# Kernel tuning notes

Hardware: AMD Instinct MI355X
Metric: run time of the kernel (lower is better)

Reference implementation:

```python
import jax, jax.numpy as jnp
import numpy as np

NUM_HEADS = 8
GROUPS = 32
EPS = 1e-5


def group_norm(x, gamma, beta):
    # x: (b, c, L)
    b, c, L = x.shape
    xg = x.reshape(b, GROUPS, c // GROUPS, L)
    mean = xg.mean(axis=(2, 3), keepdims=True)
    var = xg.var(axis=(2, 3), keepdims=True)
    xn = ((xg - mean) / jnp.sqrt(var + EPS)).reshape(b, c, L)
    return xn * gamma[None, :, None] + beta[None, :, None]


def setup_inputs() -> dict:
    key = jax.random.key(0)
    ks = jax.random.split(key, 8)
    b, c, h, w = 8, 512, 32, 32
    inner = c  # inner_channels == -1 -> channels
    x = jax.random.normal(ks[0], (b, c, h, w), dtype=jnp.float32)
    gamma = jnp.ones((c,), dtype=jnp.float32)
    beta = jnp.zeros((c,), dtype=jnp.float32)
    Wq = jax.random.normal(ks[1], (inner, c), dtype=jnp.float32) * 0.02
    bq = jnp.zeros((inner,), dtype=jnp.float32)
    Wkv = jax.random.normal(ks[2], (2 * inner, c), dtype=jnp.float32) * 0.02
    bkv = jnp.zeros((2 * inner,), dtype=jnp.float32)
    Wo = jax.random.normal(ks[3], (c, inner), dtype=jnp.float32) * 0.02
    bo = jnp.zeros((c,), dtype=jnp.float32)
    return {"x": x, "gamma": gamma, "beta": beta, "Wq": Wq, "bq": bq,
            "Wkv": Wkv, "bkv": bkv, "Wo": Wo, "bo": bo}


def reference(x, gamma, beta, Wq, bq, Wkv, bkv, Wo, bo):
    b, c = x.shape[:2]
    spatial = x.shape[2:]
    L = int(np.prod(spatial))
    inner = Wq.shape[0]
    dh = inner // NUM_HEADS
    scale = dh ** -0.5  # NOTE: applied to BOTH q and k, as in the source

    xr = x.reshape(b, c, L)
    hn = group_norm(xr, gamma, beta)          # norm(x); also serves as context

    # 1x1 Conv1d == channel matmul
    q = jnp.einsum('oc,bcl->bol', Wq, hn) + bq[None, :, None]
    kv = jnp.einsum('oc,bcl->bol', Wkv, hn) + bkv[None, :, None]
    k, v = jnp.split(kv, 2, axis=1)

    # (b, heads, dh, L)
    qh = (q * scale).reshape(b, NUM_HEADS, dh, L)
    kh = (k * scale).reshape(b, NUM_HEADS, dh, L)
    vh = v.reshape(b, NUM_HEADS, dh, L)

    dots = jnp.einsum('bhdt,bhds->bhts', qh, kh)
    attn = jax.nn.softmax(dots.astype(jnp.float32), axis=-1).astype(dots.dtype)
    out = jnp.einsum('bhts,bhds->bhdt', attn, vh)  # (b, heads, dh, L)

    out = out.reshape(b, inner, L)
    # output Linear over the channel dim
    out = jnp.einsum('oc,bcl->bol', Wo, out) + bo[None, :, None]
    return (xr + out).reshape(b, c, *spatial)
```

## Files before the change

### kernel.cpp

```cpp
#include <hip/hip_runtime.h>
#include <math.h>

#define B_ 8
#define C_ 512
#define L_ 1024
#define NH_ 8
#define DH_ 64
#define EPS 1e-5f
#define SCALE 0.125f
#define QSCALE (0.125f * 1.44269504088896f)

typedef __bf16 bf16x8 __attribute__((ext_vector_type(8)));
typedef __bf16 bf16x4 __attribute__((ext_vector_type(4)));
typedef float  f32x4  __attribute__((ext_vector_type(4)));

#define MFMA16(a, b, c) __builtin_amdgcn_mfma_f32_16x16x32_bf16((a), (b), (c), 0, 0, 0)

__device__ __forceinline__ void glds16(const __bf16* g, __bf16* l) {
    __builtin_amdgcn_global_load_lds((const __attribute__((address_space(1))) void*)(g),
                                     (__attribute__((address_space(3))) void*)(l),
                                     16, 0, 0);
}

__global__ __launch_bounds__(256)
void prep_kernel(const float* __restrict__ Wq, const float* __restrict__ Wkv,
                 const float* __restrict__ Wo, __bf16* __restrict__ dst,
                 const float* __restrict__ x, float* __restrict__ stats) {
    __shared__ float rs[256], rss[256];
    int bid = blockIdx.x, tid = threadIdx.x;
    if (bid < 1024) {
        int idx = bid * 256 + tid;
        float4 v;
        if (idx < 65536)        v = ((const float4*)Wq)[idx];
        else if (idx < 196608)  v = ((const float4*)Wkv)[idx - 65536];
        else                    v = ((const float4*)Wo)[idx - 196608];
        bf16x4 o;
        o[0] = (__bf16)v.x; o[1] = (__bf16)v.y; o[2] = (__bf16)v.z; o[3] = (__bf16)v.w;
        ((bf16x4*)dst)[idx] = o;
        return;
    }
    int bg = bid - 1024;
    size_t goff = (size_t)bg * 16 * L_;
    const float4* x4 = (const float4*)(x + goff);
    float s = 0.f, ss = 0.f;
    for (int i = tid; i < 4096; i += 256) {
        float4 v = x4[i];
        s  += v.x + v.y + v.z + v.w;
        ss += v.x * v.x + v.y * v.y + v.z * v.z + v.w * v.w;
    }
    rs[tid] = s; rss[tid] = ss;
    __syncthreads();
    for (int off = 128; off > 0; off >>= 1) {
        if (tid < off) { rs[tid] += rs[tid + off]; rss[tid] += rss[tid + off]; }
        __syncthreads();
    }
    if (tid == 0) {
        const float inv_n = 1.f / 16384.f;
        float mean = rs[0] * inv_n;
        float var  = rss[0] * inv_n - mean * mean;
        stats[bg * 2]     = mean;
        stats[bg * 2 + 1] = rsqrtf(var + EPS);
    }
}

__global__ __launch_bounds__(256)
void gn_apply_kernel(const float* __restrict__ x, const float* __restrict__ gamma,
                     const float* __restrict__ beta, const float* __restrict__ stats,
                     __bf16* __restrict__ hnT) {
    __shared__ __bf16 T[32 * 520];
    const int lt = blockIdx.x, b = blockIdx.y;
    const int tid = threadIdx.x;
    const int l0 = lt * 32;
    const int cbase = tid >> 3, fl = tid & 7;
#pragma unroll
    for (int p = 0; p < 16; ++p) {
        int cc = cbase + p * 32;
        float4 v = *(const float4*)&x[((size_t)b * C_ + cc) * L_ + l0 + fl * 4];
        int bg = b * 32 + (cc >> 4);
        float m = stats[bg * 2], rstd = stats[bg * 2 + 1];
        float ga = gamma[cc] * rstd, be = beta[cc];
        T[(fl * 4 + 0) * 520 + cc] = (__bf16)((v.x - m) * ga + be);
        T[(fl * 4 + 1) * 520 + cc] = (__bf16)((v.y - m) * ga + be);
        T[(fl * 4 + 2) * 520 + cc] = (__bf16)((v.z - m) * ga + be);
        T[(fl * 4 + 3) * 520 + cc] = (__bf16)((v.w - m) * ga + be);
    }
    __syncthreads();
    const int lrow = tid >> 6, cu = tid & 63;
#pragma unroll
    for (int pp = 0; pp < 8; ++pp) {
        int l = pp * 4 + lrow;
        bf16x8 r = *(const bf16x8*)&T[l * 520 + cu * 8];
        *(bf16x8*)&hnT[((size_t)b * L_ + l0 + l) * C_ + cu * 8] = r;
    }
}

__device__ __forceinline__
void gemm_mainloop(const __bf16* __restrict__ A, const __bf16* __restrict__ Bp,
                   __bf16* As, __bf16* Bs, f32x4 acc[4][4]) {
    const int tid = threadIdx.x;
    const int lane = tid & 63, w = tid >> 6;
    const int c = lane & 15, q = lane >> 4;
    const int wm = (w >> 1) * 64, wn = (w & 1) * 64;
    const int l8 = lane >> 3, kgsw = (lane & 7) ^ l8;

    for (int k0 = 0; k0 < 512; k0 += 64) {
#pragma unroll
        for (int i = 0; i < 4; ++i) {
            int chunk = w * 4 + i;
            int row = chunk * 8 + l8;
            glds16(A  + (size_t)row * 512 + k0 + kgsw * 8, &As[chunk * 512]);
            glds16(Bp + (size_t)row * 512 + k0 + kgsw * 8, &Bs[chunk * 512]);
        }
        __syncthreads();
#pragma unroll
        for (int ks = 0; ks < 2; ++ks) {
            const int koff = ((ks * 4 + q) ^ (c & 7)) * 8;
            bf16x8 af[4], bfr[4];
#pragma unroll
            for (int m = 0; m < 4; ++m)
                af[m] = *(const bf16x8*)&As[(wm + m * 16 + c) * 64 + koff];
#pragma unroll
            for (int n = 0; n < 4; ++n)
                bfr[n] = *(const bf16x8*)&Bs[(wn + n * 16 + c) * 64 + koff];
#pragma unroll
            for (int m = 0; m < 4; ++m)
#pragma unroll
                for (int n = 0; n < 4; ++n)
                    acc[m][n] = MFMA16(af[m], bfr[n], acc[m][n]);
        }
        __syncthreads();
    }
}

__global__ __launch_bounds__(256)
void qkv_kernel(const __bf16* __restrict__ Wq_bf, const __bf16* __restrict__ Wkv_bf,
                const __bf16* __restrict__ hnT,
                const float* __restrict__ bq, const float* __restrict__ bkv,
                __bf16* __restrict__ qT, __bf16* __restrict__ kT,
                __bf16* __restrict__ vv) {
    __shared__ __bf16 SMEM[128 * 64 * 2];
    __bf16* As = SMEM;
    __bf16* Bs = SMEM + 128 * 64;
    const int b = blockIdx.y;
    const int xx = blockIdx.x;
    const int sec = xx >> 5, t = xx & 31;
    const __bf16* hb = hnT + (size_t)b * L_ * C_;

    const __bf16 *A, *Bp;
    int m0, n0;
    if (sec < 2) {
        m0 = (t & 3) * 128; n0 = (t >> 2) * 128;
        A  = (sec == 0 ? Wq_bf : Wkv_bf) + (size_t)m0 * 512;
        Bp = hb + (size_t)n0 * 512;
    } else {
        m0 = (t >> 2) * 128; n0 = (t & 3) * 128;
        A  = hb + (size_t)m0 * 512;
        Bp = Wkv_bf + (size_t)(512 + n0) * 512;
    }

    f32x4 acc[4][4];
#pragma unroll
    for (int m = 0; m < 4; ++m)
#pragma unroll
        for (int n = 0; n < 4; ++n)
#pragma unroll
            for (int r = 0; r < 4; ++r) acc[m][n][r] = 0.f;

    gemm_mainloop(A, Bp, As, Bs, acc);

    const int tid = threadIdx.x, lane = tid & 63, w = tid >> 6;
    const int c = lane & 15, q = lane >> 4;
    const int wm = (w >> 1) * 64, wn = (w & 1) * 64;

    __bf16* T2 = SMEM;
    const float* bias = (sec == 0) ? bq : bkv;
    const float scl = (sec == 0) ? QSCALE : SCALE;
#pragma unroll
    for (int mt = 0; mt < 4; ++mt)
#pragma unroll
        for (int nt = 0; nt < 4; ++nt) {
            int n_loc = wn + nt * 16 + c;
            int u4 = (wm >> 2) + mt * 4 + q;
            int u4sw = u4 ^ ((n_loc & 7) << 1);
            bf16x4 ov;
            if (sec < 2) {
                int ob = m0 + wm + mt * 16 + q * 4;
#pragma unroll
                for (int r = 0; r < 4; ++r)
                    ov[r] = (__bf16)((acc[mt][nt][r] + bias[ob + r]) * scl);
            } else {
                float bi = bkv[512 + n0 + n_loc];
#pragma unroll
                for (int r = 0; r < 4; ++r)
                    ov[r] = (__bf16)(acc[mt][nt][r] + bi);
            }
            *(bf16x4*)&T2[n_loc * 128 + u4sw * 4] = ov;
        }
    __syncthreads();
#pragma unroll
    for (int p = 0; p < 8; ++p) {
        int rrow = p * 16 + (tid >> 4);
        int u16 = tid & 15;
        int u4p = (u16 * 2) ^ ((rrow & 7) << 1);
        bf16x8 val = *(const bf16x8*)&T2[rrow * 128 + u4p * 4];
        if (sec < 2) {
            int l = n0 + rrow;
            int og = m0 + u16 * 8;
            int hh = og >> 6, d0 = og & 63;
            __bf16* dstp = (sec == 0) ? qT : kT;
            *(bf16x8*)&dstp[((size_t)(b * NH_ + hh) * L_ + l) * DH_ + d0] = val;
        } else {
            int o = n0 + rrow;
            int lg = m0 + u16 * 8;
            *(bf16x8*)&vv[((size_t)b * C_ + o) * L_ + lg] = val;
        }
    }
}

__global__ __launch_bounds__(256)
void attn_kernel(const __bf16* __restrict__ qT, const __bf16* __restrict__ kT,
                 const __bf16* __restrict__ vv, __bf16* __restrict__ aoT) {
    const int tt = blockIdx.x, h = blockIdx.y, b = blockIdx.z;
    const int t0 = tt * 128;
    __shared__ __bf16 Qs[128 * 64];
    __shared__ __bf16 Ks[64 * 64];
    __shared__ __bf16 Vs[64 * 64];
    __shared__ __bf16 Ones[16 * 64];
    __shared__ __bf16 Ps[128 * 72];

    const int tid = threadIdx.x, lane = tid & 63, w = tid >> 6;
    const int c = lane & 15, q = lane >> 4;
    const int l8 = lane >> 3, kg = (lane & 7) ^ l8;

    const __bf16* qbase = qT + ((size_t)(b * NH_ + h) * L_ + t0) * DH_;
    const __bf16* kbase = kT + (size_t)(b * NH_ + h) * L_ * DH_;
    const __bf16* vbase = vv + (size_t)(b * C_ + h * DH_) * L_;

    {
        int row = tid >> 4, u8 = tid & 15;
        int u8sw = (((u8 >> 1) ^ (row & 7)) << 1) | (u8 & 1);
        float fv = (row == 0) ? 1.f : 0.f;
        bf16x4 val;
        val[0] = (__bf16)fv; val[1] = (__bf16)fv; val[2] = (__bf16)fv; val[3] = (__bf16)fv;
        *(bf16x4*)&Ones[row * 64 + u8sw * 4] = val;
    }
#pragma unroll
    for (int i = 0; i < 4; ++i) {
        int chunk = w * 4 + i;
        int row = chunk * 8 + l8;
        glds16(qbase + (size_t)row * DH_ + kg * 8, &Qs[chunk * 512]);
    }

    f32x4 o_acc[2][4], o_l[2];
#pragma unroll
    for (int n2 = 0; n2 < 2; ++n2) {
#pragma unroll
        for (int dt = 0; dt < 4; ++dt)
#pragma unroll
            for (int r = 0; r < 4; ++r) o_acc[n2][dt][r] = 0.f;
#pragma unroll
        for (int r = 0; r < 4; ++r) o_l[n2][r] = 0.f;
    }

    for (int s0 = 0; s0 < L_; s0 += 64) {
#pragma unroll
        for (int i = 0; i < 2; ++i) {
            int chunk = w * 2 + i;
            int row = chunk * 8 + l8;
            glds16(kbase + (size_t)(s0 + row) * DH_ + kg * 8, &Ks[chunk * 512]);
            glds16(vbase + (size_t)row * L_ + s0 + kg * 8, &Vs[chunk * 512]);
        }
        __syncthreads();

        f32x4 sres[4][2];
#pragma unroll
        for (int mt = 0; mt < 4; ++mt)
#pragma unroll
            for (int r = 0; r < 4; ++r) { sres[mt][0][r] = 0.f; sres[mt][1][r] = 0.f; }
#pragma unroll
        for (int ks = 0; ks < 2; ++ks) {
            const int koff = ((ks * 4 + q) ^ (c & 7)) * 8;
            bf16x8 bQ0 = *(const bf16x8*)&Qs[(w * 32 + c) * 64 + koff];
            bf16x8 bQ1 = *(const bf16x8*)&Qs[(w * 32 + 16 + c) * 64 + koff];
#pragma unroll
            for (int mt = 0; mt < 4; ++mt) {
                bf16x8 aK = *(const bf16x8*)&Ks[(mt * 16 + c) * 64 + koff];
                sres[mt][0] = MFMA16(aK, bQ0, sres[mt][0]);
                sres[mt][1] = MFMA16(aK, bQ1, sres[mt][1]);
            }
        }

#pragma unroll
        for (int n2 = 0; n2 < 2; ++n2) {
            int trow = w * 32 + n2 * 16 + c;
#pragma unroll
            for (int mt = 0; mt < 4; ++mt) {
                bf16x4 pv;
#pragma unroll
                for (int r = 0; r < 4; ++r) pv[r] = (__bf16)exp2f(sres[mt][n2][r]);
                *(bf16x4*)&Ps[trow * 72 + (mt * 4 + q) * 4] = pv;
            }
        }

#pragma unroll
        for (int ks = 0; ks < 2; ++ks) {
            const int koff = ((ks * 4 + q) ^ (c & 7)) * 8;
            bf16x8 aV[4];
#pragma unroll
            for (int dt = 0; dt < 4; ++dt)
                aV[dt] = *(const bf16x8*)&Vs[(dt * 16 + c) * 64 + koff];
            bf16x8 aO = *(const bf16x8*)&Ones[c * 64 + koff];
#pragma unroll
            for (int n2 = 0; n2 < 2; ++n2) {
                bf16x8 bp = *(const bf16x8*)&Ps[(w * 32 + n2 * 16 + c) * 72 + ks * 32 + q * 8];
#pragma unroll
                for (int dt = 0; dt < 4; ++dt)
                    o_acc[n2][dt] = MFMA16(aV[dt], bp, o_acc[n2][dt]);
                o_l[n2] = MFMA16(aO, bp, o_l[n2]);
            }
        }
        __syncthreads();
    }

#pragma unroll
    for (int n2 = 0; n2 < 2; ++n2) {
        float lsum = __shfl(o_l[n2][0], c);
        float linv = 1.f / lsum;
        int tg = t0 + w * 32 + n2 * 16 + c;
        __bf16* aobase = aoT + ((size_t)b * L_ + tg) * C_ + h * DH_;
#pragma unroll
        for (int dt = 0; dt < 4; ++dt) {
            bf16x4 ov;
#pragma unroll
            for (int r = 0; r < 4; ++r) ov[r] = (__bf16)(o_acc[n2][dt][r] * linv);
            *(bf16x4*)&aobase[dt * 16 + q * 4] = ov;
        }
    }
}

__global__ __launch_bounds__(256)
void proj_kernel(const __bf16* __restrict__ aoT, const __bf16* __restrict__ Wo_bf,
                 const float* __restrict__ bo, const float* __restrict__ x,
                 float* __restrict__ out) {
    __shared__ __bf16 As[128 * 64], Bs[128 * 64];
    const int b = blockIdx.y, t = blockIdx.x;
    const int m0 = (t >> 2) * 128;
    const int n0 = (t & 3) * 128;
    const __bf16* A  = aoT + (size_t)b * L_ * C_ + (size_t)m0 * 512;
    const __bf16* Bp = Wo_bf + (size_t)n0 * 512;

    f32x4 acc[4][4];
#pragma unroll
    for (int m = 0; m < 4; ++m)
#pragma unroll
        for (int n = 0; n < 4; ++n)
#pragma unroll
            for (int r = 0; r < 4; ++r) acc[m][n][r] = 0.f;

    gemm_mainloop(A, Bp, As, Bs, acc);

    const int tid = threadIdx.x, lane = tid & 63, w = tid >> 6;
    const int c = lane & 15, q = lane >> 4;
    const int wm = (w >> 1) * 64, wn = (w & 1) * 64;

#pragma unroll
    for (int mt = 0; mt < 4; ++mt)
#pragma unroll
        for (int nt = 0; nt < 4; ++nt) {
            int lb = m0 + wm + mt * 16 + q * 4;
            int o  = n0 + wn + nt * 16 + c;
            float bi = bo[o];
            size_t off = ((size_t)b * C_ + o) * L_ + lb;
            float4 xv = *(const float4*)&x[off];
            float4 rv;
            rv.x = acc[mt][nt][0] + bi + xv.x;
            rv.y = acc[mt][nt][1] + bi + xv.y;
            rv.z = acc[mt][nt][2] + bi + xv.z;
            rv.w = acc[mt][nt][3] + bi + xv.w;
            *(float4*)&out[off] = rv;
        }
}

extern "C" void kernel_launch(void* const* d_in, const int* in_sizes, int n_in,
                              void* d_out, int out_size, void* d_ws, size_t ws_size,
                              hipStream_t stream) {
    const float* x     = (const float*)d_in[0];
    const float* gamma = (const float*)d_in[1];
    const float* beta  = (const float*)d_in[2];
    const float* Wq    = (const float*)d_in[3];
    const float* bq    = (const float*)d_in[4];
    const float* Wkv   = (const float*)d_in[5];
    const float* bkv   = (const float*)d_in[6];
    const float* Wo    = (const float*)d_in[7];
    const float* bo    = (const float*)d_in[8];
    float* out = (float*)d_out;

    __bf16* wsb = (__bf16*)d_ws;
    __bf16* Wq_bf  = wsb;
    __bf16* Wkv_bf = wsb + 262144;
    __bf16* Wo_bf  = wsb + 786432;
    __bf16* hnT    = wsb + 1048576;
    __bf16* qT     = wsb + 5242880;
    __bf16* kT     = wsb + 9437184;
    __bf16* vv     = wsb + 13631488;
    __bf16* aoT    = wsb + 17825792;
    float*  stats  = (float*)(wsb + 22020096);

    prep_kernel<<<dim3(1280), 256, 0, stream>>>(Wq, Wkv, Wo, wsb, x, stats);
    gn_apply_kernel<<<dim3(32, B_), 256, 0, stream>>>(x, gamma, beta, stats, hnT);
    qkv_kernel<<<dim3(96, B_), 256, 0, stream>>>(Wq_bf, Wkv_bf, hnT, bq, bkv, qT, kT, vv);
    attn_kernel<<<dim3(8, NH_, B_), 256, 0, stream>>>(qT, kT, vv, aoT);
    proj_kernel<<<dim3(32, B_), 256, 0, stream>>>(aoT, Wo_bf, bo, x, out);
}
```

Baseline: 174.3 us.

## Double-buffer K/V tiles in attention and use 512 threads with 16 query rows per wave

The attention kernel now runs 8 waves per block, each handling 16 query rows instead of 32, and double-buffers the K and V LDS tiles so the load of tile it+2 is issued while tile it is being computed. Raw s_waitcnt/s_barrier asm replaces __syncthreads to keep one tile's loads in flight. The aim is to hide global-load latency and raise wave-level parallelism, at the cost of more LDS, more barrier traffic and K/V fragments that are no longer reused across two query subtiles per wave.

```diff
diff --git a/kernel.cpp b/kernel.cpp
--- a/kernel.cpp
+++ b/kernel.cpp
@@ -217,14 +217,14 @@
     }
 }
 
-__global__ __launch_bounds__(256)
+__global__ __launch_bounds__(512)
 void attn_kernel(const __bf16* __restrict__ qT, const __bf16* __restrict__ kT,
                  const __bf16* __restrict__ vv, __bf16* __restrict__ aoT) {
     const int tt = blockIdx.x, h = blockIdx.y, b = blockIdx.z;
     const int t0 = tt * 128;
     __shared__ __bf16 Qs[128 * 64];
-    __shared__ __bf16 Ks[64 * 64];
-    __shared__ __bf16 Vs[64 * 64];
+    __shared__ __bf16 Ks[2][64 * 64];
+    __shared__ __bf16 Vs[2][64 * 64];
     __shared__ __bf16 Ones[16 * 64];
     __shared__ __bf16 Ps[128 * 72];
 
@@ -236,7 +236,7 @@
     const __bf16* kbase = kT + (size_t)(b * NH_ + h) * L_ * DH_;
     const __bf16* vbase = vv + (size_t)(b * C_ + h * DH_) * L_;
 
-    {
+    if (tid < 256) {
         int row = tid >> 4, u8 = tid & 15;
         int u8sw = (((u8 >> 1) ^ (row & 7)) << 1) | (u8 & 1);
         float fv = (row == 0) ? 1.f : 0.f;
@@ -245,59 +245,56 @@
         *(bf16x4*)&Ones[row * 64 + u8sw * 4] = val;
     }
 #pragma unroll
-    for (int i = 0; i < 4; ++i) {
-        int chunk = w * 4 + i;
+    for (int i = 0; i < 2; ++i) {
+        int chunk = w * 2 + i;
         int row = chunk * 8 + l8;
         glds16(qbase + (size_t)row * DH_ + kg * 8, &Qs[chunk * 512]);
     }
-
-    f32x4 o_acc[2][4], o_l[2];
-#pragma unroll
-    for (int n2 = 0; n2 < 2; ++n2) {
-#pragma unroll
-        for (int dt = 0; dt < 4; ++dt)
-#pragma unroll
-            for (int r = 0; r < 4; ++r) o_acc[n2][dt][r] = 0.f;
-#pragma unroll
-        for (int r = 0; r < 4; ++r) o_l[n2][r] = 0.f;
-    }
-
-    for (int s0 = 0; s0 < L_; s0 += 64) {
-#pragma unroll
-        for (int i = 0; i < 2; ++i) {
-            int chunk = w * 2 + i;
-            int row = chunk * 8 + l8;
-            glds16(kbase + (size_t)(s0 + row) * DH_ + kg * 8, &Ks[chunk * 512]);
-            glds16(vbase + (size_t)row * L_ + s0 + kg * 8, &Vs[chunk * 512]);
-        }
-        __syncthreads();
-
-        f32x4 sres[4][2];
+    {
+        int row = w * 8 + l8;
+        glds16(kbase + (size_t)row * DH_ + kg * 8, &Ks[0][w * 512]);
+        glds16(vbase + (size_t)row * L_ + kg * 8, &Vs[0][w * 512]);
+        glds16(kbase + (size_t)(64 + row) * DH_ + kg * 8, &Ks[1][w * 512]);
+        glds16(vbase + (size_t)row * L_ + 64 + kg * 8, &Vs[1][w * 512]);
+    }
+    asm volatile("s_waitcnt vmcnt(2) lgkmcnt(0)" ::: "memory");
+    asm volatile("s_barrier" ::: "memory");
+
+    f32x4 o_acc[4], o_l;
+#pragma unroll
+    for (int dt = 0; dt < 4; ++dt)
+#pragma unroll
+        for (int r = 0; r < 4; ++r) o_acc[dt][r] = 0.f;
+#pragma unroll
+    for (int r = 0; r < 4; ++r) o_l[r] = 0.f;
+
+    for (int it = 0; it < 16; ++it) {
+        const __bf16* Kc = Ks[it & 1];
+        const __bf16* Vc = Vs[it & 1];
+
+        f32x4 sres[4];
 #pragma unroll
         for (int mt = 0; mt < 4; ++mt)
 #pragma unroll
-            for (int r = 0; r < 4; ++r) { sres[mt][0][r] = 0.f; sres[mt][1][r] = 0.f; }
+            for (int r = 0; r < 4; ++r) sres[mt][r] = 0.f;
 #pragma unroll
         for (int ks = 0; ks < 2; ++ks) {
             const int koff = ((ks * 4 + q) ^ (c & 7)) * 8;
-            bf16x8 bQ0 = *(const bf16x8*)&Qs[(w * 32 + c) * 64 + koff];
-            bf16x8 bQ1 = *(const bf16x8*)&Qs[(w * 32 + 16 + c) * 64 + koff];
+            bf16x8 bQ = *(const bf16x8*)&Qs[(w * 16 + c) * 64 + koff];
 #pragma unroll
             for (int mt = 0; mt < 4; ++mt) {
-                bf16x8 aK = *(const bf16x8*)&Ks[(mt * 16 + c) * 64 + koff];
-                sres[mt][0] = MFMA16(aK, bQ0, sres[mt][0]);
-                sres[mt][1] = MFMA16(aK, bQ1, sres[mt][1]);
+                bf16x8 aK = *(const bf16x8*)&Kc[(mt * 16 + c) * 64 + koff];
+                sres[mt] = MFMA16(aK, bQ, sres[mt]);
             }
         }
 
-#pragma unroll
-        for (int n2 = 0; n2 < 2; ++n2) {
-            int trow = w * 32 + n2 * 16 + c;
+        {
+            int trow = w * 16 + c;
 #pragma unroll
             for (int mt = 0; mt < 4; ++mt) {
                 bf16x4 pv;
 #pragma unroll
-                for (int r = 0; r < 4; ++r) pv[r] = (__bf16)exp2f(sres[mt][n2][r]);
+                for (int r = 0; r < 4; ++r) pv[r] = (__bf16)exp2f(sres[mt][r]);
                 *(bf16x4*)&Ps[trow * 72 + (mt * 4 + q) * 4] = pv;
             }
         }
@@ -305,34 +302,39 @@
 #pragma unroll
         for (int ks = 0; ks < 2; ++ks) {
             const int koff = ((ks * 4 + q) ^ (c & 7)) * 8;
-            bf16x8 aV[4];
-#pragma unroll
-            for (int dt = 0; dt < 4; ++dt)
-                aV[dt] = *(const bf16x8*)&Vs[(dt * 16 + c) * 64 + koff];
+            bf16x8 bp = *(const bf16x8*)&Ps[(w * 16 + c) * 72 + ks * 32 + q * 8];
             bf16x8 aO = *(const bf16x8*)&Ones[c * 64 + koff];
 #pragma unroll
-            for (int n2 = 0; n2 < 2; ++n2) {
-                bf16x8 bp = *(const bf16x8*)&Ps[(w * 32 + n2 * 16 + c) * 72 + ks * 32 + q * 8];
-#pragma unroll
-                for (int dt = 0; dt < 4; ++dt)
-                    o_acc[n2][dt] = MFMA16(aV[dt], bp, o_acc[n2][dt]);
-                o_l[n2] = MFMA16(aO, bp, o_l[n2]);
+            for (int dt = 0; dt < 4; ++dt) {
+                bf16x8 aV = *(const bf16x8*)&Vc[(dt * 16 + c) * 64 + koff];
+                o_acc[dt] = MFMA16(aV, bp, o_acc[dt]);
             }
-        }
-        __syncthreads();
-    }
-
-#pragma unroll
-    for (int n2 = 0; n2 < 2; ++n2) {
-        float lsum = __shfl(o_l[n2][0], c);
+            o_l = MFMA16(aO, bp, o_l);
+        }
+
+        asm volatile("s_barrier" ::: "memory");
+        if (it < 14) {
+            int s0n = (it + 2) * 64;
+            int row = w * 8 + l8;
+            glds16(kbase + (size_t)(s0n + row) * DH_ + kg * 8, &Ks[it & 1][w * 512]);
+            glds16(vbase + (size_t)row * L_ + s0n + kg * 8, &Vs[it & 1][w * 512]);
+            asm volatile("s_waitcnt vmcnt(2)" ::: "memory");
+        } else {
+            asm volatile("s_waitcnt vmcnt(0)" ::: "memory");
+        }
+        asm volatile("s_barrier" ::: "memory");
+    }
+
+    {
+        float lsum = __shfl(o_l[0], c);
         float linv = 1.f / lsum;
-        int tg = t0 + w * 32 + n2 * 16 + c;
+        int tg = t0 + w * 16 + c;
         __bf16* aobase = aoT + ((size_t)b * L_ + tg) * C_ + h * DH_;
 #pragma unroll
         for (int dt = 0; dt < 4; ++dt) {
             bf16x4 ov;
 #pragma unroll
-            for (int r = 0; r < 4; ++r) ov[r] = (__bf16)(o_acc[n2][dt][r] * linv);
+            for (int r = 0; r < 4; ++r) ov[r] = (__bf16)(o_acc[dt][r] * linv);
             *(bf16x4*)&aobase[dt * 16 + q * 4] = ov;
         }
     }
@@ -409,6 +411,6 @@
     prep_kernel<<<dim3(1280), 256, 0, stream>>>(Wq, Wkv, Wo, wsb, x, stats);
     gn_apply_kernel<<<dim3(32, B_), 256, 0, stream>>>(x, gamma, beta, stats, hnT);
     qkv_kernel<<<dim3(96, B_), 256, 0, stream>>>(Wq_bf, Wkv_bf, hnT, bq, bkv, qT, kT, vv);
-    attn_kernel<<<dim3(8, NH_, B_), 256, 0, stream>>>(qT, kT, vv, aoT);
+    attn_kernel<<<dim3(8, NH_, B_), 512, 0, stream>>>(qT, kT, vv, aoT);
     proj_kernel<<<dim3(32, B_), 256, 0, stream>>>(aoT, Wo_bf, bo, x, out);
 }
```

Result: faster. 169.5 us (-2.8%).
